# Kernel optimization log

Hardware: AMD Instinct MI355X
Metric: run time of the kernel (lower is better)

The kernel has to match this reference:

```python
import jax, jax.numpy as jnp
import numpy as np

HEADS = 8
LN_EPS = 1e-5
BN_EPS = 1e-5
MIN_EPS, MAX_EPS = 1e-4, 10.0


def _ln(x, g, b):
    m = x.mean(-1, keepdims=True)
    v = x.var(-1, keepdims=True)
    return (x - m) / jnp.sqrt(v + LN_EPS) * g + b


def _pos2d(a, b, dim, temperature=10000.0):
    # faithful to build_2d_sincos_position_embedding(w=a, h=b)
    grid_a = jnp.arange(a, dtype=jnp.float32)
    grid_b = jnp.arange(b, dtype=jnp.float32)
    ga, gb = jnp.meshgrid(grid_a, grid_b, indexing='ij')  # (a, b)
    pos_dim = dim // 4
    omega = 1.0 / (temperature ** (jnp.arange(pos_dim, dtype=jnp.float32) / pos_dim))
    out_a = ga.flatten()[:, None] * omega[None]
    out_b = gb.flatten()[:, None] * omega[None]
    return jnp.concatenate([jnp.sin(out_a), jnp.cos(out_a), jnp.sin(out_b), jnp.cos(out_b)], axis=1)  # (a*b, dim)


def _avgpool(x, k):
    bb, cc, H, W = x.shape
    return x.reshape(bb, cc, H // k, k, W // k, k).mean((3, 5))


def setup_inputs() -> dict:
    key = jax.random.key(0)
    c1, c2, bs = 256, 512, 16
    ks = jax.random.split(key, 12)

    def lin(k, o, i):
        return (jax.random.normal(k, (o, i), jnp.float32) * (1.0 / np.sqrt(i))).astype(jnp.float32)

    return {
        'a3': jax.random.normal(ks[0], (bs, c1, 80, 80), jnp.float32),
        'a4': jax.random.normal(ks[1], (bs, c2, 40, 40), jnp.float32),
        'conv_w': lin(ks[2], c1, c2), 'conv_b': jnp.zeros((c1,), jnp.float32),
        'bn_g': jnp.ones((c1,), jnp.float32), 'bn_b': jnp.zeros((c1,), jnp.float32),
        'q_w': lin(ks[3], c1, c1), 'q_b': jnp.zeros((c1,), jnp.float32),
        'q_ln_g': jnp.ones((c1,), jnp.float32), 'q_ln_b': jnp.zeros((c1,), jnp.float32),
        'k_w': lin(ks[4], c1, c1), 'k_b': jnp.zeros((c1,), jnp.float32),
        'k_ln_g': jnp.ones((c1,), jnp.float32), 'k_ln_b': jnp.zeros((c1,), jnp.float32),
        'v_w': lin(ks[5], c1, c1), 'v_b': jnp.zeros((c1,), jnp.float32),
        'out_w': lin(ks[6], c1, c1), 'out_b': jnp.zeros((c1,), jnp.float32),
        'lin1_w': lin(ks[7], 4 * c1, c1), 'lin1_b': jnp.zeros((4 * c1,), jnp.float32),
        'lin2_w': lin(ks[8], c1, 4 * c1), 'lin2_b': jnp.zeros((c1,), jnp.float32),
        'norm1_g': jnp.ones((c1,), jnp.float32), 'norm1_b': jnp.zeros((c1,), jnp.float32),
        'norm2_g': jnp.ones((c1,), jnp.float32), 'norm2_b': jnp.zeros((c1,), jnp.float32),
        'idx': 10,
    }


def reference(a3, a4, conv_w, conv_b, bn_g, bn_b, q_w, q_b, q_ln_g, q_ln_b,
              k_w, k_b, k_ln_g, k_ln_b, v_w, v_b, out_w, out_b,
              lin1_w, lin1_b, lin2_w, lin2_b, norm1_g, norm1_b, norm2_g, norm2_b, idx):
    a3 = jnp.nan_to_num(a3, nan=0.0, posinf=1e4, neginf=-1e4)
    a4 = jnp.nan_to_num(a4, nan=0.0, posinf=1e4, neginf=-1e4)
    orig_a3, orig_a4 = a3, a4

    # high_to_low_embed: 1x1 conv + BatchNorm (eval: running_mean=0, running_var=1)
    a4e = jnp.einsum('bchw,oc->bohw', a4, conv_w) + conv_b[None, :, None, None]
    a4e = a4e / jnp.sqrt(1.0 + BN_EPS) * bn_g[None, :, None, None] + bn_b[None, :, None, None]

    if idx == 10:
        a3d = _avgpool(a3, 2)
    else:
        a3d = _avgpool(a3, 4)
        a4e = _avgpool(a4e, 2)

    bs, c, h, w = a3d.shape
    tgt = h * w
    src = a4e.shape[2] * a4e.shape[3]

    residual = a3d.reshape(bs, c, tgt).transpose(0, 2, 1)      # (bs, tgt, c)
    a3f = a3d.reshape(bs, c, tgt).transpose(2, 0, 1)            # (tgt, bs, c)
    a4f = a4e.reshape(bs, c, src).transpose(2, 0, 1)            # (src, bs, c)

    pos = _pos2d(h, w, c)[:, None, :]                           # (h*w, 1, c)
    a3f = a3f + pos
    a4f = a4f + pos                                             # src == tgt by construction

    Q = jax.nn.relu(_ln(a3f @ q_w.T + q_b, q_ln_g, q_ln_b))
    K = jax.nn.relu(_ln(a4f @ k_w.T + k_b, k_ln_g, k_ln_b))
    V = a4f @ v_w.T + v_b

    hd = c // HEADS
    Q = Q.reshape(tgt, bs, HEADS, hd).transpose(1, 2, 0, 3)     # (b, h, tgt, hd)
    K = K.reshape(src, bs, HEADS, hd).transpose(1, 2, 0, 3)
    V = V.reshape(src, bs, HEADS, hd).transpose(1, 2, 0, 3)

    m = max(src, tgt)
    wi = (np.pi / 2) * jnp.arange(1, m + 1, dtype=jnp.float32) / m  # (m,)
    sq = jnp.sin(wi[:tgt])[None, None, :, None]
    cq = jnp.cos(wi[:tgt])[None, None, :, None]
    sk = jnp.sin(wi[:src])[None, None, :, None]
    ck = jnp.cos(wi[:src])[None, None, :, None]
    Q_ = jnp.concatenate([Q * sq, Q * cq], -1)                  # (b, h, tgt, 2hd)
    K_ = jnp.concatenate([K * sk, K * ck], -1)                  # (b, h, src, 2hd)

    KV = jnp.einsum('bhsd,bhse->bhde', K_, V)                   # (b, h, 2hd, hd)
    Zden = jnp.einsum('bhld,bhd->bhl', Q_, K_.sum(2))
    Z = 1.0 / jnp.clip(Zden, MIN_EPS, MAX_EPS)
    attn = jnp.einsum('bhld,bhde->bhle', Q_, KV) * Z[..., None]  # (b, h, tgt, hd)

    attn = attn.transpose(2, 0, 1, 3).reshape(tgt, bs, c)
    out = (attn @ out_w.T + out_b).transpose(1, 0, 2)           # (bs, tgt, c)
    out = _ln(out, norm1_g, norm1_b)
    out = residual + out

    res2 = out
    ff = jax.nn.gelu(out @ lin1_w.T + lin1_b, approximate=False) @ lin2_w.T + lin2_b
    ff = _ln(ff, norm2_g, norm2_b)
    out = res2 + ff

    a3_sa = out.transpose(0, 2, 1).reshape(bs, c, h, w)
    a3_sa = jax.image.resize(a3_sa, orig_a3.shape, 'bilinear')  # align_corners=False
    a3_sa = a3_sa * orig_a3

    B4, C4, H4, W4 = orig_a4.shape
    a4_up = jax.image.resize(orig_a4, (B4, C4, 2 * H4, 2 * W4), 'bilinear')
    return (a3_sa, a4_up)
```

## Files before the change

### kernel.cpp

```cpp
#include <hip/hip_runtime.h>
#include <math.h>


typedef __attribute__((ext_vector_type(8))) short bf16x8;
typedef __attribute__((ext_vector_type(8))) unsigned short us8;
typedef __attribute__((ext_vector_type(4))) unsigned short us4h;
typedef __attribute__((ext_vector_type(4))) float f32x4;

__device__ __forceinline__ unsigned short f2bf(float f) {
  unsigned int u = __float_as_uint(f);
  u += 0x7fff + ((u >> 16) & 1);
  return (unsigned short)(u >> 16);
}
__device__ __forceinline__ float bf2f(unsigned short u) {
  return __uint_as_float(((unsigned int)u) << 16);
}

__device__ __forceinline__ void gload16(const void* g, void* l) {
  __builtin_amdgcn_global_load_lds(
      (const __attribute__((address_space(1))) void*)g,
      (__attribute__((address_space(3))) void*)l, 16, 0, 0);
}

__global__ __launch_bounds__(256) void prep_kernel(
    const float* __restrict__ cw, const float* __restrict__ qw,
    const float* __restrict__ kw, const float* __restrict__ vw,
    const float* __restrict__ ow, const float* __restrict__ l1w,
    const float* __restrict__ l2w, unsigned short* __restrict__ wbf,
    float* __restrict__ pos,
    const float* __restrict__ a4, unsigned short* __restrict__ a4t) {
  __shared__ float buf[64][65];
  if (blockIdx.x < 448) {
    int gid = blockIdx.x * 256 + threadIdx.x;
    size_t e0 = (size_t)gid * 8;
    const float* src; size_t off;
    if (e0 < 131072)      { src = cw;  off = e0; }
    else if (e0 < 196608) { src = qw;  off = e0 - 131072; }
    else if (e0 < 262144) { src = kw;  off = e0 - 196608; }
    else if (e0 < 327680) { src = vw;  off = e0 - 262144; }
    else if (e0 < 393216) { src = ow;  off = e0 - 327680; }
    else if (e0 < 655360) { src = l1w; off = e0 - 393216; }
    else                  { src = l2w; off = e0 - 655360; }
    float4 v0 = *(const float4*)(src + off);
    float4 v1 = *(const float4*)(src + off + 4);
    us8 r;
    r[0] = f2bf(v0.x); r[1] = f2bf(v0.y); r[2] = f2bf(v0.z); r[3] = f2bf(v0.w);
    r[4] = f2bf(v1.x); r[5] = f2bf(v1.y); r[6] = f2bf(v1.z); r[7] = f2bf(v1.w);
    *(us8*)(wbf + e0) = r;
  } else if (blockIdx.x < 2048) {
    int s = blockIdx.x - 448, c = threadIdx.x;
    int y = s / 40, x = s - y * 40;
    int quad = c >> 6, i = c & 63;
    float omega = expf(-(float)i * (9.2103403719761836f / 64.0f));
    float coord = (quad < 2) ? (float)y : (float)x;
    float a = coord * omega;
    pos[s * 256 + c] = (quad & 1) ? cosf(a) : sinf(a);
  } else {
    int id = blockIdx.x - 2048;
    int b = id / 200;
    int r = id - b * 200;
    int s0 = (r % 25) * 64, k0 = (r / 25) * 64;
    const float* src = a4 + ((size_t)b * 512 + k0) * 1600 + s0;
#pragma unroll
    for (int p = 0; p < 4; ++p) {
      int idx = p * 256 + threadIdx.x;
      int kk = idx >> 4, s4 = (idx & 15) * 4;
      float4 v = *(const float4*)(src + (size_t)kk * 1600 + s4);
      buf[kk][s4 + 0] = v.x; buf[kk][s4 + 1] = v.y;
      buf[kk][s4 + 2] = v.z; buf[kk][s4 + 3] = v.w;
    }
    __syncthreads();
    unsigned short* dst = a4t + ((size_t)b * 1600 + s0) * 512 + k0;
#pragma unroll
    for (int p = 0; p < 4; ++p) {
      int idx = p * 256 + threadIdx.x;
      int ss = idx >> 4, kq = (idx & 15) * 4;
      us4h v;
      v[0] = f2bf(buf[kq + 0][ss]); v[1] = f2bf(buf[kq + 1][ss]);
      v[2] = f2bf(buf[kq + 2][ss]); v[3] = f2bf(buf[kq + 3][ss]);
      *(us4h*)(dst + (size_t)ss * 512 + kq) = v;
    }
  }
}

__global__ __launch_bounds__(640) void avgpool_kernel(
    const float* __restrict__ a3, const float* __restrict__ pos,
    unsigned short* __restrict__ X3) {
  __shared__ float buf2[256][44];
  int y = blockIdx.x, b = blockIdx.y;
  int tid = threadIdx.x;
  int x2 = tid % 20, cq = tid / 20;
#pragma unroll
  for (int it = 0; it < 8; ++it) {
    int c = cq + 32 * it;
    const float* p = a3 + (((size_t)(b * 256 + c) * 80 + 2 * y) * 80 + x2 * 4);
    float4 r0 = *(const float4*)p;
    float4 r1 = *(const float4*)(p + 80);
    buf2[c][2 * x2]     = 0.25f * ((r0.x + r0.y) + (r1.x + r1.y));
    buf2[c][2 * x2 + 1] = 0.25f * ((r0.z + r0.w) + (r1.z + r1.w));
  }
  __syncthreads();
  size_t t0 = (size_t)b * 1600 + y * 40;
  int sbase = y * 40;
#pragma unroll
  for (int it = 0; it < 4; ++it) {
    int idx = it * 640 + tid;
    int c = idx & 255, xq = idx >> 8;
    int x0 = xq * 4;
    float4 v = *(const float4*)&buf2[c][x0];
#pragma unroll
    for (int j = 0; j < 4; ++j) {
      float pv = pos[(size_t)(sbase + x0 + j) * 256 + c];
      float vv = (j == 0) ? v.x : (j == 1) ? v.y : (j == 2) ? v.z : v.w;
      X3[(t0 + x0 + j) * 256 + c] = f2bf(vv + pv);
    }
  }
}

struct __align__(16) SmemT {
  unsigned short Albs[2][64][32];
  unsigned short Wlds[2][256][32];
  float part[4][64][2];
};

template<int EPI>
__device__ __forceinline__ void gemm_body(
    SmemT& S,
    const unsigned short* __restrict__ A, const unsigned short* __restrict__ W,
    const float* __restrict__ bias, void* __restrict__ outp,
    const int K, const int ldN, int t0, int o0,
    const float* __restrict__ posb,
    const float* __restrict__ g1, const float* __restrict__ b1,
    const unsigned short* __restrict__ res) {
  int tid = threadIdx.x;
  int lane = tid & 63, w = tid >> 6;
  int mw = w >> 2, nw = w & 3;
  int g = lane >> 4, cl = lane & 15;
  f32x4 acc[2][4] = {};

  int lrow = lane >> 2, lchk = lane & 3;
  const unsigned short* ag = A + (size_t)(t0 + (w >> 1) * 16 + lrow) * K
                               + (w & 1) * 32 + lchk * 8;
  unsigned short* al = &S.Albs[w & 1][(w >> 1) * 16][0];
  const unsigned short* wg[4];
  unsigned short* wl[4];
#pragma unroll
  for (int j = 0; j < 4; ++j) {
    int u = w * 4 + j;
    int kk = u & 1, rb = u >> 1;
    wg[j] = W + (size_t)(o0 + rb * 16 + lrow) * K + kk * 32 + lchk * 8;
    wl[j] = &S.Wlds[kk][rb * 16][0];
  }

  for (int k0 = 0; k0 < K; k0 += 64) {
    __syncthreads();
    gload16(ag + k0, al);
#pragma unroll
    for (int j = 0; j < 4; ++j) gload16(wg[j] + k0, wl[j]);
    __syncthreads();
#pragma unroll
    for (int kk = 0; kk < 2; ++kk) {
      bf16x8 af[2], bw[4];
#pragma unroll
      for (int ms = 0; ms < 2; ++ms)
        af[ms] = *(const bf16x8*)&S.Albs[kk][mw * 32 + ms * 16 + cl][g * 8];
#pragma unroll
      for (int ns = 0; ns < 4; ++ns)
        bw[ns] = *(const bf16x8*)&S.Wlds[kk][nw * 64 + ns * 16 + cl][g * 8];
#pragma unroll
      for (int ms = 0; ms < 2; ++ms)
#pragma unroll
        for (int ns = 0; ns < 4; ++ns)
          acc[ms][ns] = __builtin_amdgcn_mfma_f32_16x16x32_bf16(af[ms], bw[ns], acc[ms][ns], 0, 0, 0);
    }
  }

  float bv[4];
#pragma unroll
  for (int ns = 0; ns < 4; ++ns) bv[ns] = bias[o0 + nw * 64 + ns * 16 + cl];
  int sbase = t0 % 1600;

  if constexpr (EPI == 2 || EPI == 3 || EPI == 5) {
#pragma unroll
    for (int ms = 0; ms < 2; ++ms) {
#pragma unroll
      for (int i = 0; i < 4; ++i) {
        float p = 0.f, q = 0.f;
#pragma unroll
        for (int ns = 0; ns < 4; ++ns) {
          float v = acc[ms][ns][i] + bv[ns];
          p += v; q += v * v;
        }
        p += __shfl_xor(p, 1); q += __shfl_xor(q, 1);
        p += __shfl_xor(p, 2); q += __shfl_xor(q, 2);
        p += __shfl_xor(p, 4); q += __shfl_xor(q, 4);
        p += __shfl_xor(p, 8); q += __shfl_xor(q, 8);
        if (cl == 0) {
          int rl = mw * 32 + ms * 16 + g * 4 + i;
          S.part[nw][rl][0] = p;
          S.part[nw][rl][1] = q;
        }
      }
    }
    __syncthreads();
  }

  if constexpr (EPI == 5) {
    float* of = (float*)outp;
    int bb = t0 / 1600;
#pragma unroll
    for (int ms = 0; ms < 2; ++ms) {
      int rl0 = mw * 32 + ms * 16 + g * 4;
      float mean[4], inv[4];
#pragma unroll
      for (int i = 0; i < 4; ++i) {
        float sp = (S.part[0][rl0 + i][0] + S.part[1][rl0 + i][0]) +
                   (S.part[2][rl0 + i][0] + S.part[3][rl0 + i][0]);
        float sq = (S.part[0][rl0 + i][1] + S.part[1][rl0 + i][1]) +
                   (S.part[2][rl0 + i][1] + S.part[3][rl0 + i][1]);
        mean[i] = sp * (1.f / 256.f);
        float var = sq * (1.f / 256.f) - mean[i] * mean[i];
        inv[i] = rsqrtf(var + 1e-5f);
      }
#pragma unroll
      for (int ns = 0; ns < 4; ++ns) {
        int col = nw * 64 + ns * 16 + cl;
        float gg = g1[col], b2 = b1[col];
        float4 y;
#pragma unroll
        for (int i = 0; i < 4; ++i) {
          float v = acc[ms][ns][i] + bv[ns];
          float yy = (v - mean[i]) * inv[i] * gg + b2;
          yy += bf2f(res[(size_t)(t0 + rl0 + i) * 256 + col]);
          if (i == 0) y.x = yy; else if (i == 1) y.y = yy;
          else if (i == 2) y.z = yy; else y.w = yy;
        }
        *(float4*)(of + ((size_t)(bb * 256 + col) * 1600) + sbase + rl0) = y;
      }
    }
    return;
  }

  unsigned short* ob = (unsigned short*)outp;
#pragma unroll
  for (int ms = 0; ms < 2; ++ms) {
#pragma unroll
    for (int i = 0; i < 4; ++i) {
      int rl = mw * 32 + ms * 16 + g * 4 + i;
      int t = t0 + rl;
      float mean = 0.f, inv = 0.f;
      if constexpr (EPI == 2 || EPI == 3) {
        float sp = (S.part[0][rl][0] + S.part[1][rl][0]) + (S.part[2][rl][0] + S.part[3][rl][0]);
        float sq = (S.part[0][rl][1] + S.part[1][rl][1]) + (S.part[2][rl][1] + S.part[3][rl][1]);
        mean = sp * (1.f / 256.f);
        float var = sq * (1.f / 256.f) - mean * mean;
        inv = rsqrtf(var + 1e-5f);
      }
#pragma unroll
      for (int ns = 0; ns < 4; ++ns) {
        int col = nw * 64 + ns * 16 + cl;
        float v = acc[ms][ns][i] + bv[ns];
        size_t oidx = (size_t)t * ldN + o0 + col;
        if constexpr (EPI == 0) {
          ob[oidx] = f2bf(v);
        } else if constexpr (EPI == 1) {
          const float is = 0.99999500003749968f;
          float y = v * (is * g1[col]) + b1[col] + posb[(size_t)(sbase + rl) * 256 + col];
          ob[oidx] = f2bf(y);
        } else if constexpr (EPI == 2) {
          float y = (v - mean) * inv * g1[col] + b1[col];
          ob[oidx] = f2bf(fmaxf(y, 0.f));
        } else if constexpr (EPI == 3) {
          float y = (v - mean) * inv * g1[col] + b1[col];
          y += bf2f(res[(size_t)t * 256 + col]) - posb[(size_t)(sbase + rl) * 256 + col];
          ob[oidx] = f2bf(y);
        } else if constexpr (EPI == 4) {
          float y = 0.5f * v * (1.f + erff(v * 0.7071067811865475f));
          ob[oidx] = f2bf(y);
        }
      }
    }
  }
}

template<int EPI>
__global__ __launch_bounds__(512) void fgemm(
    const unsigned short* __restrict__ A, const unsigned short* __restrict__ W,
    const float* __restrict__ bias, void* __restrict__ outp,
    const int K, const int ldN,
    const float* __restrict__ posb,
    const float* __restrict__ g1, const float* __restrict__ b1,
    const unsigned short* __restrict__ res) {
  __shared__ SmemT S;
  gemm_body<EPI>(S, A, W, bias, outp, K, ldN, blockIdx.x * 64, blockIdx.y * 256,
                 posb, g1, b1, res);
}

__global__ __launch_bounds__(512) void qkv_kernel(
    const unsigned short* __restrict__ X3b, const unsigned short* __restrict__ X4b,
    const unsigned short* __restrict__ w_q, const unsigned short* __restrict__ w_k,
    const unsigned short* __restrict__ w_v,
    const float* __restrict__ q_b, const float* __restrict__ k_b, const float* __restrict__ v_b,
    const float* __restrict__ q_g, const float* __restrict__ q_bt,
    const float* __restrict__ k_g, const float* __restrict__ k_bt,
    unsigned short* __restrict__ Qo, unsigned short* __restrict__ Ko,
    unsigned short* __restrict__ Vo) {
  __shared__ SmemT S;
  int t0 = blockIdx.x * 64;
  if (blockIdx.y == 0) {
    gemm_body<2>(S, X3b, w_q, q_b, Qo, 256, 256, t0, 0, nullptr, q_g, q_bt, nullptr);
  } else if (blockIdx.y == 1) {
    gemm_body<2>(S, X4b, w_k, k_b, Ko, 256, 256, t0, 0, nullptr, k_g, k_bt, nullptr);
  } else {
    gemm_body<0>(S, X4b, w_v, v_b, Vo, 256, 256, t0, 0, nullptr, nullptr, nullptr, nullptr);
  }
}

__global__ __launch_bounds__(256) void kv_kernel(
    const unsigned short* __restrict__ Kb, const unsigned short* __restrict__ Vb,
    float* __restrict__ KVp, float* __restrict__ Ksp) {
  __shared__ float Kc[64][32];
  __shared__ float Vc[64][32];
  __shared__ float sv[64], cv[64];
  __shared__ float red[4][64];
  int bx = blockIdx.x;
  int bh = bx / 5, sp = bx - bh * 5;
  int b = bh >> 3, h = bh & 7;
  int tid = threadIdx.x;
  int e = tid & 31, dg = tid >> 5;
  int d4 = dg * 4;
  int dks = tid & 63, partid = tid >> 6;
  float accs[4] = {0.f, 0.f, 0.f, 0.f};
  float accc[4] = {0.f, 0.f, 0.f, 0.f};
  float ks = 0.f;
  size_t base = ((size_t)b * 1600) * 256 + h * 32;
  for (int s0 = sp * 320; s0 < sp * 320 + 320; s0 += 64) {
    __syncthreads();
#pragma unroll
    for (int p = 0; p < 8; ++p) {
      int si = dg + p * 8;
      Kc[si][e] = bf2f(Kb[base + (size_t)(s0 + si) * 256 + e]);
      Vc[si][e] = bf2f(Vb[base + (size_t)(s0 + si) * 256 + e]);
    }
    if (tid < 64) {
      float wv = 1.5707963267948966f * (float)(s0 + tid + 1) * (1.0f / 1600.0f);
      sv[tid] = sinf(wv);
      cv[tid] = cosf(wv);
    }
    __syncthreads();
#pragma unroll 8
    for (int si = 0; si < 64; ++si) {
      float vv = Vc[si][e];
      float sn = sv[si], cs = cv[si];
      float4 k4 = *(const float4*)&Kc[si][d4];
      float p0 = k4.x * vv, p1 = k4.y * vv, p2 = k4.z * vv, p3 = k4.w * vv;
      accs[0] = fmaf(p0, sn, accs[0]); accc[0] = fmaf(p0, cs, accc[0]);
      accs[1] = fmaf(p1, sn, accs[1]); accc[1] = fmaf(p1, cs, accc[1]);
      accs[2] = fmaf(p2, sn, accs[2]); accc[2] = fmaf(p2, cs, accc[2]);
      accs[3] = fmaf(p3, sn, accs[3]); accc[3] = fmaf(p3, cs, accc[3]);
    }
#pragma unroll 4
    for (int q = 0; q < 16; ++q) {
      int si = partid * 16 + q;
      float kvv = (dks < 32) ? Kc[si][dks] * sv[si] : Kc[si][dks - 32] * cv[si];
      ks += kvv;
    }
  }
  red[partid][dks] = ks;
  __syncthreads();
  size_t ob = (size_t)sp * 128 + bh;
  if (tid < 64)
    Ksp[ob * 64 + tid] = (red[0][tid] + red[1][tid]) + (red[2][tid] + red[3][tid]);
#pragma unroll
  for (int i = 0; i < 4; ++i) {
    KVp[ob * 2048 + (d4 + i) * 32 + e] = accs[i];
    KVp[ob * 2048 + (32 + d4 + i) * 32 + e] = accc[i];
  }
}

__global__ __launch_bounds__(256) void kvred_kernel(
    const float* __restrict__ KVp, const float* __restrict__ Ksp,
    float* __restrict__ KV, float* __restrict__ Ks) {
  int bh = blockIdx.x, tid = threadIdx.x;
  size_t o = (size_t)bh * 2048 + tid * 8;
  float4 s0 = make_float4(0, 0, 0, 0), s1 = make_float4(0, 0, 0, 0);
#pragma unroll
  for (int sp = 0; sp < 5; ++sp) {
    const float* p = KVp + ((size_t)sp * 128 + bh) * 2048 + tid * 8;
    float4 a = *(const float4*)p;
    float4 b2 = *(const float4*)(p + 4);
    s0.x += a.x; s0.y += a.y; s0.z += a.z; s0.w += a.w;
    s1.x += b2.x; s1.y += b2.y; s1.z += b2.z; s1.w += b2.w;
  }
  *(float4*)(KV + o) = s0;
  *(float4*)(KV + o + 4) = s1;
  if (tid < 64) {
    float t = 0.f;
#pragma unroll
    for (int sp = 0; sp < 5; ++sp) t += Ksp[((size_t)sp * 128 + bh) * 64 + tid];
    Ks[bh * 64 + tid] = t;
  }
}

__global__ __launch_bounds__(256) void attn_kernel(
    const unsigned short* __restrict__ Qb, const float* __restrict__ KV,
    const float* __restrict__ Ksum, unsigned short* __restrict__ attn) {
  int grp = threadIdx.x >> 5;
  int e = threadIdx.x & 31;
  int t = blockIdx.x * 8 + grp;
  int b = t / 1600, s = t - b * 1600;
  float wv = 1.5707963267948966f * (float)(s + 1) * (1.0f / 1600.0f);
  float sq = sinf(wv), cq = cosf(wv);
  const unsigned short* qrow = Qb + (size_t)t * 256;
  for (int h = 0; h < 8; ++h) {
    int bh = b * 8 + h;
    const float* kv = KV + (size_t)bh * 2048;
    const float* ksm = Ksum + (size_t)bh * 64;
    float qe = bf2f(qrow[h * 32 + e]);
    float zp = qe * (sq * ksm[e] + cq * ksm[32 + e]);
    zp += __shfl_xor(zp, 1); zp += __shfl_xor(zp, 2);
    zp += __shfl_xor(zp, 4); zp += __shfl_xor(zp, 8); zp += __shfl_xor(zp, 16);
    float acc = 0.f;
#pragma unroll 8
    for (int d = 0; d < 32; ++d) {
      float qv = bf2f(qrow[h * 32 + d]);
      acc = fmaf(qv * sq, kv[d * 32 + e], acc);
      acc = fmaf(qv * cq, kv[(32 + d) * 32 + e], acc);
    }
    float zc = fminf(fmaxf(zp, 1e-4f), 10.0f);
    attn[(size_t)t * 256 + h * 32 + e] = f2bf(acc * (1.0f / zc));
  }
}

__device__ __forceinline__ float4 up_row4(const float* sm, int Y, int q) {
  float fy = Y * 0.5f - 0.25f;
  int iy = (int)floorf(fy);
  float dy = fy - (float)iy;
  int y0 = iy < 0 ? 0 : iy;
  int y1 = (iy + 1) > 39 ? 39 : (iy + 1);
  const float* r0 = sm + y0 * 40;
  const float* r1 = sm + y1 * 40;
  int cm1 = (2 * q - 1) < 0 ? 0 : (2 * q - 1);
  int cp2 = (2 * q + 2) > 39 ? 39 : (2 * q + 2);
  float w1 = 1.f - dy;
  float s0 = w1 * r0[cm1]       + dy * r1[cm1];
  float s1 = w1 * r0[2 * q]     + dy * r1[2 * q];
  float s2 = w1 * r0[2 * q + 1] + dy * r1[2 * q + 1];
  float s3 = w1 * r0[cp2]       + dy * r1[cp2];
  float4 o;
  o.x = 0.25f * s0 + 0.75f * s1;
  o.y = 0.75f * s1 + 0.25f * s2;
  o.z = 0.25f * s1 + 0.75f * s2;
  o.w = 0.75f * s2 + 0.25f * s3;
  return o;
}

__global__ __launch_bounds__(256) void upsample_fused_kernel(
    const float* __restrict__ a3p, const float* __restrict__ a3,
    const float* __restrict__ a4, float* __restrict__ out0,
    float* __restrict__ out1) {
  __shared__ float sm[1600];
  int id = blockIdx.x;
  const float* src;
  float* outp;
  const float* mul = nullptr;
  if (id < 4096) {
    int c = id & 255, b = id >> 8;
    src = a3p + ((size_t)b * 256 + c) * 1600;
    outp = out0 + ((size_t)b * 256 + c) * 6400;
    mul = a3 + ((size_t)b * 256 + c) * 6400;
  } else {
    int id2 = id - 4096;
    int c = id2 & 511, b = id2 >> 9;
    src = a4 + ((size_t)b * 512 + c) * 1600;
    outp = out1 + ((size_t)b * 512 + c) * 6400;
  }
  for (int i = threadIdx.x; i < 400; i += 256)
    *(float4*)&sm[i * 4] = *(const float4*)(src + i * 4);
  __syncthreads();
  if (mul) {
    for (int i = threadIdx.x; i < 1600; i += 256) {
      int Y = i / 20, q = i - Y * 20;
      float4 o = up_row4(sm, Y, q);
      float4 m = *(const float4*)(mul + i * 4);
      o.x *= m.x; o.y *= m.y; o.z *= m.z; o.w *= m.w;
      *(float4*)(outp + i * 4) = o;
    }
  } else {
    for (int i = threadIdx.x; i < 1600; i += 256) {
      int Y = i / 20, q = i - Y * 20;
      float4 o = up_row4(sm, Y, q);
      *(float4*)(outp + i * 4) = o;
    }
  }
}

extern "C" void kernel_launch(void* const* d_in, const int* in_sizes, int n_in,
                              void* d_out, int out_size, void* d_ws, size_t ws_size,
                              hipStream_t stream) {
  const float* a3     = (const float*)d_in[0];
  const float* a4     = (const float*)d_in[1];
  const float* conv_w = (const float*)d_in[2];
  const float* conv_b = (const float*)d_in[3];
  const float* bn_g   = (const float*)d_in[4];
  const float* bn_b   = (const float*)d_in[5];
  const float* q_w    = (const float*)d_in[6];
  const float* q_b    = (const float*)d_in[7];
  const float* q_ln_g = (const float*)d_in[8];
  const float* q_ln_b = (const float*)d_in[9];
  const float* k_w    = (const float*)d_in[10];
  const float* k_b    = (const float*)d_in[11];
  const float* k_ln_g = (const float*)d_in[12];
  const float* k_ln_b = (const float*)d_in[13];
  const float* v_w    = (const float*)d_in[14];
  const float* v_b    = (const float*)d_in[15];
  const float* out_w  = (const float*)d_in[16];
  const float* out_b  = (const float*)d_in[17];
  const float* lin1_w = (const float*)d_in[18];
  const float* lin1_b = (const float*)d_in[19];
  const float* lin2_w = (const float*)d_in[20];
  const float* lin2_b = (const float*)d_in[21];
  const float* n1_g   = (const float*)d_in[22];
  const float* n1_b   = (const float*)d_in[23];
  const float* n2_g   = (const float*)d_in[24];
  const float* n2_b   = (const float*)d_in[25];
  (void)in_sizes; (void)n_in; (void)out_size; (void)ws_size;

  float* ws = (float*)d_ws;
  float* pos  = ws + 0;
  unsigned short* wbf = (unsigned short*)(ws + 409600);
  float* KV   = ws + 868352;
  float* Ks   = ws + 1130496;
  float* KVp  = ws + 1138688;
  float* Ksp  = ws + 2449408;
  unsigned short* X3b  = (unsigned short*)(ws + 2490368);
  unsigned short* X4b  = (unsigned short*)(ws + 5767168);
  unsigned short* Qbb  = (unsigned short*)(ws + 9043968);
  unsigned short* Kbb  = (unsigned short*)(ws + 12320768);
  unsigned short* Vbb  = (unsigned short*)(ws + 15597568);
  unsigned short* o1b  = (unsigned short*)(ws + 18874368);
  unsigned short* a4tb = (unsigned short*)(ws + 22151168);
  unsigned short* ffhb = (unsigned short*)(ws + 22151168);
  float* a3p  = ws + 9043968;

  const unsigned short* w_conv = wbf;
  const unsigned short* w_q    = wbf + 131072;
  const unsigned short* w_k    = wbf + 196608;
  const unsigned short* w_v    = wbf + 262144;
  const unsigned short* w_o    = wbf + 327680;
  const unsigned short* w_l1   = wbf + 393216;
  const unsigned short* w_l2   = wbf + 655360;

  float* out0 = (float*)d_out;
  float* out1f = out0 + (size_t)16 * 256 * 80 * 80;

  prep_kernel<<<5248, 256, 0, stream>>>(conv_w, q_w, k_w, v_w, out_w, lin1_w, lin2_w,
                                        wbf, pos, a4, a4tb);
  avgpool_kernel<<<dim3(40, 16), 640, 0, stream>>>(a3, pos, X3b);
  fgemm<1><<<dim3(400, 1), 512, 0, stream>>>(a4tb, w_conv, conv_b, X4b, 512, 256, pos, bn_g, bn_b, nullptr);
  qkv_kernel<<<dim3(400, 3), 512, 0, stream>>>(X3b, X4b, w_q, w_k, w_v,
      q_b, k_b, v_b, q_ln_g, q_ln_b, k_ln_g, k_ln_b, Qbb, Kbb, Vbb);
  kv_kernel<<<640, 256, 0, stream>>>(Kbb, Vbb, KVp, Ksp);
  kvred_kernel<<<128, 256, 0, stream>>>(KVp, Ksp, KV, Ks);
  attn_kernel<<<3200, 256, 0, stream>>>(Qbb, KV, Ks, Kbb );
  fgemm<3><<<dim3(400, 1), 512, 0, stream>>>(Kbb, w_o, out_b, o1b, 256, 256, pos, n1_g, n1_b, X3b);
  fgemm<4><<<dim3(400, 4), 512, 0, stream>>>(o1b, w_l1, lin1_b, ffhb, 256, 1024, nullptr, nullptr, nullptr, nullptr);
  fgemm<5><<<dim3(400, 1), 512, 0, stream>>>(ffhb, w_l2, lin2_b, a3p, 1024, 256, nullptr, n2_g, n2_b, o1b);
  upsample_fused_kernel<<<12288, 256, 0, stream>>>(a3p, a3, a4, out0, out1f);
}
```

Baseline: 370.0 us.

## Fuse conv projection with K/V GEMMs and store pre-upsample activations in bf16

The conv+BN+pos projection of a4 is fused with the K and V projection GEMMs in one kernel. The projected tile stays in LDS, so the X4b round trip through global memory and one launch are removed, and Q gets its own GEMM launch. The final LN output that feeds the upsample is now written as bf16 instead of fp32, halving that intermediate's traffic at some precision cost. The fused kernel does three GEMMs serially per block with 400 blocks, which gives less parallelism than the previous 400x3 grid and uses more LDS per block.

```diff
diff --git a/kernel.cpp b/kernel.cpp
--- a/kernel.cpp
+++ b/kernel.cpp
@@ -206,7 +206,7 @@
   }
 
   if constexpr (EPI == 5) {
-    float* of = (float*)outp;
+    unsigned short* ob2 = (unsigned short*)outp;
     int bb = t0 / 1600;
 #pragma unroll
     for (int ms = 0; ms < 2; ++ms) {
@@ -226,16 +226,15 @@
       for (int ns = 0; ns < 4; ++ns) {
         int col = nw * 64 + ns * 16 + cl;
         float gg = g1[col], b2 = b1[col];
-        float4 y;
+        us4h y;
 #pragma unroll
         for (int i = 0; i < 4; ++i) {
           float v = acc[ms][ns][i] + bv[ns];
           float yy = (v - mean[i]) * inv[i] * gg + b2;
           yy += bf2f(res[(size_t)(t0 + rl0 + i) * 256 + col]);
-          if (i == 0) y.x = yy; else if (i == 1) y.y = yy;
-          else if (i == 2) y.z = yy; else y.w = yy;
-        }
-        *(float4*)(of + ((size_t)(bb * 256 + col) * 1600) + sbase + rl0) = y;
+          y[i] = f2bf(yy);
+        }
+        *(us4h*)(ob2 + ((size_t)(bb * 256 + col) * 1600) + sbase + rl0) = y;
       }
     }
     return;
@@ -263,10 +262,6 @@
         size_t oidx = (size_t)t * ldN + o0 + col;
         if constexpr (EPI == 0) {
           ob[oidx] = f2bf(v);
-        } else if constexpr (EPI == 1) {
-          const float is = 0.99999500003749968f;
-          float y = v * (is * g1[col]) + b1[col] + posb[(size_t)(sbase + rl) * 256 + col];
-          ob[oidx] = f2bf(y);
         } else if constexpr (EPI == 2) {
           float y = (v - mean) * inv * g1[col] + b1[col];
           ob[oidx] = f2bf(fmaxf(y, 0.f));
@@ -296,23 +291,204 @@
                  posb, g1, b1, res);
 }
 
-__global__ __launch_bounds__(512) void qkv_kernel(
-    const unsigned short* __restrict__ X3b, const unsigned short* __restrict__ X4b,
-    const unsigned short* __restrict__ w_q, const unsigned short* __restrict__ w_k,
-    const unsigned short* __restrict__ w_v,
-    const float* __restrict__ q_b, const float* __restrict__ k_b, const float* __restrict__ v_b,
-    const float* __restrict__ q_g, const float* __restrict__ q_bt,
+__global__ __launch_bounds__(512) void convkv_kernel(
+    const unsigned short* __restrict__ a4tb, const unsigned short* __restrict__ w_conv,
+    const unsigned short* __restrict__ w_k, const unsigned short* __restrict__ w_v,
+    const float* __restrict__ conv_b, const float* __restrict__ k_b,
+    const float* __restrict__ v_b,
+    const float* __restrict__ bn_g, const float* __restrict__ bn_b,
+    const float* __restrict__ posb,
     const float* __restrict__ k_g, const float* __restrict__ k_bt,
-    unsigned short* __restrict__ Qo, unsigned short* __restrict__ Ko,
-    unsigned short* __restrict__ Vo) {
+    unsigned short* __restrict__ Ko, unsigned short* __restrict__ Vo) {
   __shared__ SmemT S;
+  __shared__ unsigned short X4L[4][2][64][32];
+  int tid = threadIdx.x;
+  int lane = tid & 63, w = tid >> 6;
+  int mw = w >> 2, nw = w & 3;
+  int g = lane >> 4, cl = lane & 15;
+  int lrow = lane >> 2, lchk = lane & 3;
   int t0 = blockIdx.x * 64;
-  if (blockIdx.y == 0) {
-    gemm_body<2>(S, X3b, w_q, q_b, Qo, 256, 256, t0, 0, nullptr, q_g, q_bt, nullptr);
-  } else if (blockIdx.y == 1) {
-    gemm_body<2>(S, X4b, w_k, k_b, Ko, 256, 256, t0, 0, nullptr, k_g, k_bt, nullptr);
-  } else {
-    gemm_body<0>(S, X4b, w_v, v_b, Vo, 256, 256, t0, 0, nullptr, nullptr, nullptr, nullptr);
+  int sbase = t0 % 1600;
+  f32x4 acc[2][4] = {};
+
+  {
+    const unsigned short* ag = a4tb + (size_t)(t0 + (w >> 1) * 16 + lrow) * 512
+                                    + (w & 1) * 32 + lchk * 8;
+    unsigned short* al = &S.Albs[w & 1][(w >> 1) * 16][0];
+    const unsigned short* wg[4];
+    unsigned short* wl[4];
+#pragma unroll
+    for (int j = 0; j < 4; ++j) {
+      int u = w * 4 + j;
+      int kk = u & 1, rb = u >> 1;
+      wg[j] = w_conv + (size_t)(rb * 16 + lrow) * 512 + kk * 32 + lchk * 8;
+      wl[j] = &S.Wlds[kk][rb * 16][0];
+    }
+    for (int k0 = 0; k0 < 512; k0 += 64) {
+      __syncthreads();
+      gload16(ag + k0, al);
+#pragma unroll
+      for (int j = 0; j < 4; ++j) gload16(wg[j] + k0, wl[j]);
+      __syncthreads();
+#pragma unroll
+      for (int kk = 0; kk < 2; ++kk) {
+        bf16x8 af[2], bw[4];
+#pragma unroll
+        for (int ms = 0; ms < 2; ++ms)
+          af[ms] = *(const bf16x8*)&S.Albs[kk][mw * 32 + ms * 16 + cl][g * 8];
+#pragma unroll
+        for (int ns = 0; ns < 4; ++ns)
+          bw[ns] = *(const bf16x8*)&S.Wlds[kk][nw * 64 + ns * 16 + cl][g * 8];
+#pragma unroll
+        for (int ms = 0; ms < 2; ++ms)
+#pragma unroll
+          for (int ns = 0; ns < 4; ++ns)
+            acc[ms][ns] = __builtin_amdgcn_mfma_f32_16x16x32_bf16(af[ms], bw[ns], acc[ms][ns], 0, 0, 0);
+      }
+    }
+    const float is = 0.99999500003749968f;
+#pragma unroll
+    for (int ns = 0; ns < 4; ++ns) {
+      int col = nw * 64 + ns * 16 + cl;
+      float bvv = conv_b[col];
+      float gg = is * bn_g[col], b2 = bn_b[col];
+      int c64off = ns * 16 + cl;
+#pragma unroll
+      for (int ms = 0; ms < 2; ++ms) {
+#pragma unroll
+        for (int i = 0; i < 4; ++i) {
+          int rl = mw * 32 + ms * 16 + g * 4 + i;
+          float v = acc[ms][ns][i] + bvv;
+          float y = v * gg + b2 + posb[(size_t)(sbase + rl) * 256 + col];
+          X4L[nw][c64off >> 5][rl][c64off & 31] = f2bf(y);
+        }
+      }
+    }
+    __syncthreads();
+  }
+
+  {
+#pragma unroll
+    for (int ms = 0; ms < 2; ++ms)
+#pragma unroll
+      for (int ns = 0; ns < 4; ++ns)
+        acc[ms][ns] = (f32x4){0.f, 0.f, 0.f, 0.f};
+    for (int c = 0; c < 4; ++c) {
+      __syncthreads();
+#pragma unroll
+      for (int j = 0; j < 4; ++j) {
+        int u = w * 4 + j;
+        int kk = u & 1, rb = u >> 1;
+        gload16(w_k + (size_t)(rb * 16 + lrow) * 256 + c * 64 + kk * 32 + lchk * 8,
+                &S.Wlds[kk][rb * 16][0]);
+      }
+      __syncthreads();
+#pragma unroll
+      for (int kk = 0; kk < 2; ++kk) {
+        bf16x8 af[2], bw[4];
+#pragma unroll
+        for (int ms = 0; ms < 2; ++ms)
+          af[ms] = *(const bf16x8*)&X4L[c][kk][mw * 32 + ms * 16 + cl][g * 8];
+#pragma unroll
+        for (int ns = 0; ns < 4; ++ns)
+          bw[ns] = *(const bf16x8*)&S.Wlds[kk][nw * 64 + ns * 16 + cl][g * 8];
+#pragma unroll
+        for (int ms = 0; ms < 2; ++ms)
+#pragma unroll
+          for (int ns = 0; ns < 4; ++ns)
+            acc[ms][ns] = __builtin_amdgcn_mfma_f32_16x16x32_bf16(af[ms], bw[ns], acc[ms][ns], 0, 0, 0);
+      }
+    }
+    float bv[4];
+#pragma unroll
+    for (int ns = 0; ns < 4; ++ns) bv[ns] = k_b[nw * 64 + ns * 16 + cl];
+#pragma unroll
+    for (int ms = 0; ms < 2; ++ms) {
+#pragma unroll
+      for (int i = 0; i < 4; ++i) {
+        float p = 0.f, q = 0.f;
+#pragma unroll
+        for (int ns = 0; ns < 4; ++ns) {
+          float v = acc[ms][ns][i] + bv[ns];
+          p += v; q += v * v;
+        }
+        p += __shfl_xor(p, 1); q += __shfl_xor(q, 1);
+        p += __shfl_xor(p, 2); q += __shfl_xor(q, 2);
+        p += __shfl_xor(p, 4); q += __shfl_xor(q, 4);
+        p += __shfl_xor(p, 8); q += __shfl_xor(q, 8);
+        if (cl == 0) {
+          int rl = mw * 32 + ms * 16 + g * 4 + i;
+          S.part[nw][rl][0] = p;
+          S.part[nw][rl][1] = q;
+        }
+      }
+    }
+    __syncthreads();
+#pragma unroll
+    for (int ms = 0; ms < 2; ++ms) {
+#pragma unroll
+      for (int i = 0; i < 4; ++i) {
+        int rl = mw * 32 + ms * 16 + g * 4 + i;
+        float sp = (S.part[0][rl][0] + S.part[1][rl][0]) + (S.part[2][rl][0] + S.part[3][rl][0]);
+        float sq = (S.part[0][rl][1] + S.part[1][rl][1]) + (S.part[2][rl][1] + S.part[3][rl][1]);
+        float mean = sp * (1.f / 256.f);
+        float var = sq * (1.f / 256.f) - mean * mean;
+        float inv = rsqrtf(var + 1e-5f);
+#pragma unroll
+        for (int ns = 0; ns < 4; ++ns) {
+          int col = nw * 64 + ns * 16 + cl;
+          float v = acc[ms][ns][i] + bv[ns];
+          float y = (v - mean) * inv * k_g[col] + k_bt[col];
+          Ko[(size_t)(t0 + rl) * 256 + col] = f2bf(fmaxf(y, 0.f));
+        }
+      }
+    }
+  }
+
+  {
+#pragma unroll
+    for (int ms = 0; ms < 2; ++ms)
+#pragma unroll
+      for (int ns = 0; ns < 4; ++ns)
+        acc[ms][ns] = (f32x4){0.f, 0.f, 0.f, 0.f};
+    for (int c = 0; c < 4; ++c) {
+      __syncthreads();
+#pragma unroll
+      for (int j = 0; j < 4; ++j) {
+        int u = w * 4 + j;
+        int kk = u & 1, rb = u >> 1;
+        gload16(w_v + (size_t)(rb * 16 + lrow) * 256 + c * 64 + kk * 32 + lchk * 8,
+                &S.Wlds[kk][rb * 16][0]);
+      }
+      __syncthreads();
+#pragma unroll
+      for (int kk = 0; kk < 2; ++kk) {
+        bf16x8 af[2], bw[4];
+#pragma unroll
+        for (int ms = 0; ms < 2; ++ms)
+          af[ms] = *(const bf16x8*)&X4L[c][kk][mw * 32 + ms * 16 + cl][g * 8];
+#pragma unroll
+        for (int ns = 0; ns < 4; ++ns)
+          bw[ns] = *(const bf16x8*)&S.Wlds[kk][nw * 64 + ns * 16 + cl][g * 8];
+#pragma unroll
+        for (int ms = 0; ms < 2; ++ms)
+#pragma unroll
+          for (int ns = 0; ns < 4; ++ns)
+            acc[ms][ns] = __builtin_amdgcn_mfma_f32_16x16x32_bf16(af[ms], bw[ns], acc[ms][ns], 0, 0, 0);
+      }
+    }
+#pragma unroll
+    for (int ns = 0; ns < 4; ++ns) {
+      int col = nw * 64 + ns * 16 + cl;
+      float bvv = v_b[col];
+#pragma unroll
+      for (int ms = 0; ms < 2; ++ms)
+#pragma unroll
+        for (int i = 0; i < 4; ++i) {
+          int rl = mw * 32 + ms * 16 + g * 4 + i;
+          Vo[(size_t)(t0 + rl) * 256 + col] = f2bf(acc[ms][ns][i] + bvv);
+        }
+    }
   }
 }
 
@@ -456,29 +632,22 @@
 }
 
 __global__ __launch_bounds__(256) void upsample_fused_kernel(
-    const float* __restrict__ a3p, const float* __restrict__ a3,
+    const unsigned short* __restrict__ a3p, const float* __restrict__ a3,
     const float* __restrict__ a4, float* __restrict__ out0,
     float* __restrict__ out1) {
   __shared__ float sm[1600];
   int id = blockIdx.x;
-  const float* src;
-  float* outp;
-  const float* mul = nullptr;
   if (id < 4096) {
     int c = id & 255, b = id >> 8;
-    src = a3p + ((size_t)b * 256 + c) * 1600;
-    outp = out0 + ((size_t)b * 256 + c) * 6400;
-    mul = a3 + ((size_t)b * 256 + c) * 6400;
-  } else {
-    int id2 = id - 4096;
-    int c = id2 & 511, b = id2 >> 9;
-    src = a4 + ((size_t)b * 512 + c) * 1600;
-    outp = out1 + ((size_t)b * 512 + c) * 6400;
-  }
-  for (int i = threadIdx.x; i < 400; i += 256)
-    *(float4*)&sm[i * 4] = *(const float4*)(src + i * 4);
-  __syncthreads();
-  if (mul) {
+    const unsigned short* src = a3p + ((size_t)b * 256 + c) * 1600;
+    float* outp = out0 + ((size_t)b * 256 + c) * 6400;
+    const float* mul = a3 + ((size_t)b * 256 + c) * 6400;
+    for (int i = threadIdx.x; i < 200; i += 256) {
+      us8 v = *(const us8*)(src + i * 8);
+#pragma unroll
+      for (int j = 0; j < 8; ++j) sm[i * 8 + j] = bf2f(v[j]);
+    }
+    __syncthreads();
     for (int i = threadIdx.x; i < 1600; i += 256) {
       int Y = i / 20, q = i - Y * 20;
       float4 o = up_row4(sm, Y, q);
@@ -487,6 +656,13 @@
       *(float4*)(outp + i * 4) = o;
     }
   } else {
+    int id2 = id - 4096;
+    int c = id2 & 511, b = id2 >> 9;
+    const float* src = a4 + ((size_t)b * 512 + c) * 1600;
+    float* outp = out1 + ((size_t)b * 512 + c) * 6400;
+    for (int i = threadIdx.x; i < 400; i += 256)
+      *(float4*)&sm[i * 4] = *(const float4*)(src + i * 4);
+    __syncthreads();
     for (int i = threadIdx.x; i < 1600; i += 256) {
       int Y = i / 20, q = i - Y * 20;
       float4 o = up_row4(sm, Y, q);
@@ -534,14 +710,13 @@
   float* KVp  = ws + 1138688;
   float* Ksp  = ws + 2449408;
   unsigned short* X3b  = (unsigned short*)(ws + 2490368);
-  unsigned short* X4b  = (unsigned short*)(ws + 5767168);
   unsigned short* Qbb  = (unsigned short*)(ws + 9043968);
   unsigned short* Kbb  = (unsigned short*)(ws + 12320768);
   unsigned short* Vbb  = (unsigned short*)(ws + 15597568);
   unsigned short* o1b  = (unsigned short*)(ws + 18874368);
   unsigned short* a4tb = (unsigned short*)(ws + 22151168);
   unsigned short* ffhb = (unsigned short*)(ws + 22151168);
-  float* a3p  = ws + 9043968;
+  unsigned short* a3p  = (unsigned short*)(ws + 9043968);
 
   const unsigned short* w_conv = wbf;
   const unsigned short* w_q    = wbf + 131072;
@@ -557,9 +732,9 @@
   prep_kernel<<<5248, 256, 0, stream>>>(conv_w, q_w, k_w, v_w, out_w, lin1_w, lin2_w,
                                         wbf, pos, a4, a4tb);
   avgpool_kernel<<<dim3(40, 16), 640, 0, stream>>>(a3, pos, X3b);
-  fgemm<1><<<dim3(400, 1), 512, 0, stream>>>(a4tb, w_conv, conv_b, X4b, 512, 256, pos, bn_g, bn_b, nullptr);
-  qkv_kernel<<<dim3(400, 3), 512, 0, stream>>>(X3b, X4b, w_q, w_k, w_v,
-      q_b, k_b, v_b, q_ln_g, q_ln_b, k_ln_g, k_ln_b, Qbb, Kbb, Vbb);
+  convkv_kernel<<<400, 512, 0, stream>>>(a4tb, w_conv, w_k, w_v,
+      conv_b, k_b, v_b, bn_g, bn_b, pos, k_ln_g, k_ln_b, Kbb, Vbb);
+  fgemm<2><<<dim3(400, 1), 512, 0, stream>>>(X3b, w_q, q_b, Qbb, 256, 256, nullptr, q_ln_g, q_ln_b, nullptr);
   kv_kernel<<<640, 256, 0, stream>>>(Kbb, Vbb, KVp, Ksp);
   kvred_kernel<<<128, 256, 0, stream>>>(KVp, Ksp, KV, Ks);
   attn_kernel<<<3200, 256, 0, stream>>>(Qbb, KV, Ks, Kbb );
```

After: 373.0 us. Within noise of the previous version (+0.8%).
